# Optimization experiments

Hardware: AMD Instinct MI355X
Metric: run time of the kernel (lower is better)

The kernel has to match this reference:

```python
import jax, jax.numpy as jnp
import numpy as np

EPS = 1e-5  # torch BatchNorm default


def setup_inputs() -> dict:
    key = jax.random.key(0)
    k1, k2, k3 = jax.random.split(key, 3)
    N, C, T, V, O = 64, 64, 300, 25, 64
    x = jax.random.normal(k1, (N, C, T, V), dtype=jnp.float32)
    # 24 = V-1 convs, each (O, C, 1, 2) -> packed as (V-1, O, C, 2), scaled like conv_init
    W = jax.random.normal(k2, (V - 1, O, C, 2), dtype=jnp.float32) * (1.0 / np.sqrt(2 * C))
    b = jax.random.normal(k3, (V - 1, O), dtype=jnp.float32) * 0.01
    gamma = jnp.ones((O,), dtype=jnp.float32)
    beta = jnp.zeros((O,), dtype=jnp.float32)
    return {"x": x, "W": W, "b": b, "gamma": gamma, "beta": beta}


def reference(x, W, b, gamma, beta):
    # x: (N, C, T, V); W: (V-1, O, C, 2); b: (V-1, O)
    # Math of the original loop: out[..., v] = sum_i W0_i @ x[..., v]
    #   + sum_i W1_i @ x[..., (v+i+1) % V] + sum_i b_i
    V = x.shape[-1]
    W0 = W[..., 0]  # (V-1, O, C)
    W1 = W[..., 1]  # (V-1, O, C)
    # identity-tap term: all W0 share the same column -> sum once
    S0 = W0.sum(axis=0)  # (O, C)
    out = jnp.einsum('oc,nctv->notv', S0, x)
    # circular term: source u = (v+i+1)%V  <=>  i = (u-v-1)%V, valid for u != v
    v_idx = jnp.arange(V)
    off = (v_idx[None, :] - v_idx[:, None] - 1) % V  # (V_target, V_source) -> i, equals V-1 when u==v
    W1p = jnp.concatenate([W1, jnp.zeros_like(W1[:1])], axis=0)  # index V-1 maps to zero (u==v excluded)
    Wg = W1p[off]  # (V, V, O, C), zero on the diagonal
    out = out + jnp.einsum('vuoc,nctu->notv', Wg, x)
    out = out + b.sum(axis=0)[None, :, None, None]
    # BatchNorm2d (training-mode batch stats, biased variance) + ReLU
    mean = out.mean(axis=(0, 2, 3), keepdims=True)
    var = out.var(axis=(0, 2, 3), keepdims=True)
    out = (out - mean) * jax.lax.rsqrt(var + EPS)
    out = out * gamma[None, :, None, None] + beta[None, :, None, None]
    return jax.nn.relu(out)
```

## Files before the change

### kernel.cpp

```cpp
#include <hip/hip_runtime.h>


typedef short  s16x8 __attribute__((ext_vector_type(8)));
typedef float  f32x4 __attribute__((ext_vector_type(4)));

#define NTHR_   256
#define RPB_    250
#define NBR_    30
#define TS_     260

__device__ __forceinline__ unsigned short f2bf(float f) {
  unsigned u = __builtin_bit_cast(unsigned, f);
  return (unsigned short)((u + 0x7FFFu + ((u >> 16) & 1u)) >> 16);
}

__global__ void pack_w_kernel(const float* __restrict__ W, s16x8* __restrict__ Wg) {
  int idx = blockIdx.x * 256 + threadIdx.x;
  if (idx >= 12800) return;
  int lane  = idx & 63;
  int ni    = (idx >> 6) & 3;
  int chunk = (idx >> 8) & 1;
  int s     = idx >> 9;
  int o     = (ni << 4) + (lane & 15);
  int cbase = (chunk << 5) + ((lane >> 4) << 3);
  s16x8 h;
#pragma unroll
  for (int j = 0; j < 8; ++j) {
    int c = cbase + j;
    float val;
    if (s == 0) {
      val = 0.f;
      for (int i = 0; i < 24; ++i) val += W[((i * 64 + o) * 64 + c) * 2];
    } else {
      val = W[(((s - 1) * 64 + o) * 64 + c) * 2 + 1];
    }
    h[j] = (short)f2bf(val);
  }
  Wg[idx] = h;
}

#define ADV(J) { bool w_ = (u[J] == 24); u[J] = w_ ? 0 : u[J] + 1; \
                 aoc[J] += w_ ? -384 : 16; }
#define MM(RT, CT, AF, BF) \
  acc[RT][CT] = __builtin_amdgcn_mfma_f32_16x16x32_bf16(AF, BF, acc[RT][CT], 0, 0, 0);

#define SHIFT(S_, BB)                                                          \
  {                                                                            \
    int sc_ = (S_) + 2; sc_ = (sc_ > 24) ? 24 : sc_;                           \
    const s16x8* ws_ = Wg + sc_ * 512;                                         \
    s16x8 Br0_ = ws_[tid], Br1_ = ws_[256 + tid];                              \
    const char* bq_ = Bsh + (BB) * 8192 + 4096 + (lane << 4);                  \
    __builtin_amdgcn_s_setprio(1);                                             \
    Aq0 = *(const s16x8*)(Ash + aoc[0] + 16384);                               \
    MM(0, 0, Ap0, Bp0) MM(0, 1, Ap0, Bp1)                                      \
    Bq0 = *(const s16x8*)(bq_);                                                \
    MM(0, 2, Ap0, Bp2) MM(0, 3, Ap0, Bp3)                                      \
    Aq1 = *(const s16x8*)(Ash + aoc[1] + 16384);                               \
    MM(1, 0, Ap1, Bp0) MM(1, 1, Ap1, Bp1)                                      \
    Bq1 = *(const s16x8*)(bq_ + 1024);                                         \
    MM(1, 2, Ap1, Bp2) MM(1, 3, Ap1, Bp3)                                      \
    Aq2 = *(const s16x8*)(Ash + aoc[2] + 16384);                               \
    MM(2, 0, Ap2, Bp0) MM(2, 1, Ap2, Bp1)                                      \
    Bq2 = *(const s16x8*)(bq_ + 2048);                                         \
    MM(2, 2, Ap2, Bp2) MM(2, 3, Ap2, Bp3)                                      \
    Aq3 = *(const s16x8*)(Ash + aoc[3] + 16384);                               \
    MM(3, 0, Ap3, Bp0) MM(3, 1, Ap3, Bp1)                                      \
    Bq3 = *(const s16x8*)(bq_ + 3072);                                         \
    MM(3, 2, Ap3, Bp2) MM(3, 3, Ap3, Bp3)                                      \
    __builtin_amdgcn_s_setprio(0);                                             \
    __syncthreads();                                                           \
    const char* bp_ = Bsh + (((BB) ^ 1) * 8192) + (lane << 4);                 \
    __builtin_amdgcn_s_setprio(1);                                             \
    ADV(0) Ap0 = *(const s16x8*)(Ash + aoc[0]);                                \
    MM(0, 0, Aq0, Bq0) MM(0, 1, Aq0, Bq1)                                      \
    Bp0 = *(const s16x8*)(bp_);                                                \
    MM(0, 2, Aq0, Bq2) MM(0, 3, Aq0, Bq3)                                      \
    ADV(1) Ap1 = *(const s16x8*)(Ash + aoc[1]);                                \
    MM(1, 0, Aq1, Bq0) MM(1, 1, Aq1, Bq1)                                      \
    Bp1 = *(const s16x8*)(bp_ + 1024);                                         \
    MM(1, 2, Aq1, Bq2) MM(1, 3, Aq1, Bq3)                                      \
    ADV(2) Ap2 = *(const s16x8*)(Ash + aoc[2]);                                \
    MM(2, 0, Aq2, Bq0) MM(2, 1, Aq2, Bq1)                                      \
    Bp2 = *(const s16x8*)(bp_ + 2048);                                         \
    MM(2, 2, Aq2, Bq2) MM(2, 3, Aq2, Bq3)                                      \
    ADV(3) Ap3 = *(const s16x8*)(Ash + aoc[3]);                                \
    MM(3, 0, Aq3, Bq0) MM(3, 1, Aq3, Bq1)                                      \
    Bp3 = *(const s16x8*)(bp_ + 3072);                                         \
    MM(3, 2, Aq3, Bq2) MM(3, 3, Aq3, Bq3)                                      \
    __builtin_amdgcn_s_setprio(0);                                             \
    *(s16x8*)(Bsh + (BB) * 8192 + (tid << 4)) = Br0_;                          \
    *(s16x8*)(Bsh + (BB) * 8192 + 4096 + (tid << 4)) = Br1_;                   \
  }

__global__ __launch_bounds__(NTHR_) void tap_mm_kernel(
    const float* __restrict__ x, const s16x8* __restrict__ Wg,
    float* __restrict__ out, float* __restrict__ partials) {
  __shared__ __align__(16) char Ash[32768];
  __shared__ __align__(16) char Bsh[16384];
  float* red2 = (float*)Bsh;
  int br = blockIdx.x, n = blockIdx.y;
  int r0 = br * RPB_;
  const float* xn = x + n * 480000 + r0;
  int tid = threadIdx.x;
  int wid = tid >> 6, lane = tid & 63;
  int l15 = lane & 15, lk = lane >> 4;

  s16x8 p0 = Wg[tid], p1 = Wg[256 + tid], p2 = Wg[512 + tid], p3 = Wg[768 + tid];

#pragma unroll 2
  for (int it = 0; it < 8; ++it) {
    bool vld = tid < RPB_;
    s16x8 h;
#pragma unroll
    for (int j = 0; j < 8; ++j) {
      float f = vld ? xn[((it << 3) + j) * 7500 + tid] : 0.f;
      h[j] = (short)f2bf(f);
    }
    *(s16x8*)(Ash + (it << 12) + (tid << 4)) = h;
  }
  *(s16x8*)(Bsh + (tid << 4))         = p0;
  *(s16x8*)(Bsh + 4096 + (tid << 4))  = p1;
  *(s16x8*)(Bsh + 8192 + (tid << 4))  = p2;
  *(s16x8*)(Bsh + 12288 + (tid << 4)) = p3;

  int u[4], aoc[4];
#pragma unroll
  for (int rt = 0; rt < 4; ++rt) {
    int srow = (wid << 6) + (rt << 4) + l15;
    u[rt]   = srow % 25;
    aoc[rt] = (lk << 12) + (srow << 4);
  }
  f32x4 acc[4][4];
#pragma unroll
  for (int rt = 0; rt < 4; ++rt)
#pragma unroll
    for (int ct = 0; ct < 4; ++ct) acc[rt][ct] = (f32x4){0.f, 0.f, 0.f, 0.f};

  __syncthreads();

  s16x8 Ap0 = *(const s16x8*)(Ash + aoc[0]);
  s16x8 Ap1 = *(const s16x8*)(Ash + aoc[1]);
  s16x8 Ap2 = *(const s16x8*)(Ash + aoc[2]);
  s16x8 Ap3 = *(const s16x8*)(Ash + aoc[3]);
  const char* b0_ = Bsh + (lane << 4);
  s16x8 Bp0 = *(const s16x8*)(b0_);
  s16x8 Bp1 = *(const s16x8*)(b0_ + 1024);
  s16x8 Bp2 = *(const s16x8*)(b0_ + 2048);
  s16x8 Bp3 = *(const s16x8*)(b0_ + 3072);
  s16x8 Aq0, Aq1, Aq2, Aq3, Bq0, Bq1, Bq2, Bq3;

  for (int k = 0; k < 12; ++k) {
    SHIFT(2 * k, 0)
    SHIFT(2 * k + 1, 1)
  }
  SHIFT(24, 0)

  __syncthreads();

  float s1v[4] = {0.f, 0.f, 0.f, 0.f}, s2v[4] = {0.f, 0.f, 0.f, 0.f};
#pragma unroll
  for (int rt = 0; rt < 4; ++rt) {
#pragma unroll
    for (int qq = 0; qq < 4; ++qq) {
      int rloc = (wid << 6) + (rt << 4) + (lk << 2) + qq;
      if (rloc < RPB_) {
#pragma unroll
        for (int ct = 0; ct < 4; ++ct) {
          float val = acc[rt][ct][qq];
          s1v[ct] += val;
          s2v[ct] += val * val;
        }
      }
    }
  }
#pragma unroll
  for (int ct = 0; ct < 4; ++ct) {
    float a = s1v[ct], b = s2v[ct];
    a += __shfl_xor(a, 16); a += __shfl_xor(a, 32);
    b += __shfl_xor(b, 16); b += __shfl_xor(b, 32);
    if (lane < 16) {
      int base = ((((wid << 2) + ct) << 4) + l15) * 2;
      red2[base]     = a;
      red2[base + 1] = b;
    }
  }

  float* T = (float*)Ash;
  float* outb = out + n * 480000 + r0;
#pragma unroll
  for (int qt = 0; qt < 4; ++qt) {
    __syncthreads();
#pragma unroll
    for (int rt = 0; rt < 4; ++rt) {
      int row0 = (wid << 6) + (rt << 4) + (lk << 2);
      *(f32x4*)&T[l15 * TS_ + row0] = acc[rt][qt];
    }
    __syncthreads();
    if (qt == 0 && tid < 128) {
      int o = tid >> 1, m = tid & 1;
      int ct = o >> 4, ol = o & 15;
      float sres = 0.f;
#pragma unroll
      for (int w = 0; w < 4; ++w)
        sres += red2[((((w << 2) + ct) << 4) + ol) * 2 + m];
      int bl = n * NBR_ + br;
      partials[bl * 128 + m * 64 + o] = sres;
    }
#pragma unroll
    for (int it = 0; it < 8; ++it) {
      int idx = tid + it * NTHR_;
      if (idx < 2000) {
        int ol = idx / 125, r2 = idx - ol * 125;
        *(float2*)&outb[((qt << 4) + ol) * 7500 + (r2 << 1)] =
            *(float2*)&T[ol * TS_ + (r2 << 1)];
      }
    }
  }
}

__global__ void finalize_kernel(const float* __restrict__ part,
                                const float* __restrict__ gamma,
                                const float* __restrict__ beta,
                                float* __restrict__ scsh) {
  __shared__ float sm[512];
  int o = blockIdx.x;
  int tid = threadIdx.x;
  float s1 = 0.f, s2 = 0.f;
  for (int b = tid; b < 64 * NBR_; b += 256) {
    s1 += part[b * 128 + o];
    s2 += part[b * 128 + 64 + o];
  }
  sm[tid] = s1; sm[256 + tid] = s2;
  __syncthreads();
  for (int st = 128; st >= 1; st >>= 1) {
    if (tid < st) { sm[tid] += sm[tid + st]; sm[256 + tid] += sm[256 + tid + st]; }
    __syncthreads();
  }
  if (tid == 0) {
    const float inv = 1.0f / 480000.0f;
    float mean = sm[0] * inv;
    float var  = sm[256] * inv - mean * mean;
    float sc = gamma[o] * rsqrtf(var + 1e-5f);
    float sh = beta[o] - mean * sc;
    scsh[o]      = sc;
    scsh[64 + o] = sh;
  }
}

__global__ void bn_relu_kernel(float4* __restrict__ out, const float* __restrict__ scsh) {
  int i = blockIdx.x * blockDim.x + threadIdx.x;
  const int total = 7680000;
  int stride = gridDim.x * blockDim.x;
  for (; i < total; i += stride) {
    int o = (i / 1875) & 63;
    float sc = scsh[o], sh = scsh[64 + o];
    float4 v = out[i];
    v.x = fmaxf(fmaf(v.x, sc, sh), 0.f);
    v.y = fmaxf(fmaf(v.y, sc, sh), 0.f);
    v.z = fmaxf(fmaf(v.z, sc, sh), 0.f);
    v.w = fmaxf(fmaf(v.w, sc, sh), 0.f);
    out[i] = v;
  }
}

extern "C" void kernel_launch(void* const* d_in, const int* in_sizes, int n_in,
                              void* d_out, int out_size, void* d_ws, size_t ws_size,
                              hipStream_t stream) {
  const float* x     = (const float*)d_in[0];
  const float* W     = (const float*)d_in[1];
  const float* gamma = (const float*)d_in[3];
  const float* beta  = (const float*)d_in[4];
  float* out = (float*)d_out;

  char* ws = (char*)d_ws;
  s16x8* Wg       = (s16x8*)ws;
  float* partials = (float*)(ws + 204800);
  float* scsh     = (float*)(ws + 204800 + 983040);

  pack_w_kernel<<<dim3(50), dim3(256), 0, stream>>>(W, Wg);
  tap_mm_kernel<<<dim3(NBR_, 64), dim3(NTHR_), 0, stream>>>(x, Wg, out, partials);
  finalize_kernel<<<dim3(64), dim3(256), 0, stream>>>(partials, gamma, beta, scsh);
  bn_relu_kernel<<<dim3(2048), dim3(256), 0, stream>>>((float4*)out, scsh);
}
```

Before: 178.5 us.

## Switch tap GEMM to 32x32x16 bf16 MFMA tiles with repacked weights

```diff
diff --git a/kernel.cpp b/kernel.cpp
--- a/kernel.cpp
+++ b/kernel.cpp
@@ -1,13 +1,14 @@
 #include <hip/hip_runtime.h>
 
 
-typedef short  s16x8 __attribute__((ext_vector_type(8)));
-typedef float  f32x4 __attribute__((ext_vector_type(4)));
+typedef short  s16x8  __attribute__((ext_vector_type(8)));
+typedef float  f32x4  __attribute__((ext_vector_type(4)));
+typedef float  f32x16 __attribute__((ext_vector_type(16)));
 
 #define NTHR_   256
 #define RPB_    250
 #define NBR_    30
-#define TS_     260
+#define TS_     252
 
 __device__ __forceinline__ unsigned short f2bf(float f) {
   unsigned u = __builtin_bit_cast(unsigned, f);
@@ -17,22 +18,23 @@
 __global__ void pack_w_kernel(const float* __restrict__ W, s16x8* __restrict__ Wg) {
   int idx = blockIdx.x * 256 + threadIdx.x;
   if (idx >= 12800) return;
-  int lane  = idx & 63;
-  int ni    = (idx >> 6) & 3;
-  int chunk = (idx >> 8) & 1;
-  int s     = idx >> 9;
-  int o     = (ni << 4) + (lane & 15);
-  int cbase = (chunk << 5) + ((lane >> 4) << 3);
+  int lane = idx & 63;
+  int rest = idx >> 6;
+  int ct   = rest & 1;
+  int ks   = (rest >> 1) & 3;
+  int s    = rest >> 3;
+  int o    = (ct << 5) + (lane & 31);
+  int kb   = (ks << 4) + ((lane >> 5) << 3);
   s16x8 h;
 #pragma unroll
   for (int j = 0; j < 8; ++j) {
-    int c = cbase + j;
+    int k = kb + j;
     float val;
     if (s == 0) {
       val = 0.f;
-      for (int i = 0; i < 24; ++i) val += W[((i * 64 + o) * 64 + c) * 2];
+      for (int i = 0; i < 24; ++i) val += W[((i * 64 + o) * 64 + k) * 2];
     } else {
-      val = W[(((s - 1) * 64 + o) * 64 + c) * 2 + 1];
+      val = W[(((s - 1) * 64 + o) * 64 + k) * 2 + 1];
     }
     h[j] = (short)f2bf(val);
   }
@@ -41,52 +43,54 @@
 
 #define ADV(J) { bool w_ = (u[J] == 24); u[J] = w_ ? 0 : u[J] + 1; \
                  aoc[J] += w_ ? -384 : 16; }
-#define MM(RT, CT, AF, BF) \
-  acc[RT][CT] = __builtin_amdgcn_mfma_f32_16x16x32_bf16(AF, BF, acc[RT][CT], 0, 0, 0);
-
-#define SHIFT(S_, BB)                                                          \
+#define MM32(RT, CT, AF, BF) \
+  acc[RT][CT] = __builtin_amdgcn_mfma_f32_32x32x16_bf16(AF, BF, acc[RT][CT], 0, 0, 0);
+
+#define SHIFT32(S_, BB)                                                        \
   {                                                                            \
     int sc_ = (S_) + 2; sc_ = (sc_ > 24) ? 24 : sc_;                           \
     const s16x8* ws_ = Wg + sc_ * 512;                                         \
     s16x8 Br0_ = ws_[tid], Br1_ = ws_[256 + tid];                              \
     const char* bq_ = Bsh + (BB) * 8192 + 4096 + (lane << 4);                  \
     __builtin_amdgcn_s_setprio(1);                                             \
-    Aq0 = *(const s16x8*)(Ash + aoc[0] + 16384);                               \
-    MM(0, 0, Ap0, Bp0) MM(0, 1, Ap0, Bp1)                                      \
-    Bq0 = *(const s16x8*)(bq_);                                                \
-    MM(0, 2, Ap0, Bp2) MM(0, 3, Ap0, Bp3)                                      \
-    Aq1 = *(const s16x8*)(Ash + aoc[1] + 16384);                               \
-    MM(1, 0, Ap1, Bp0) MM(1, 1, Ap1, Bp1)                                      \
-    Bq1 = *(const s16x8*)(bq_ + 1024);                                         \
-    MM(1, 2, Ap1, Bp2) MM(1, 3, Ap1, Bp3)                                      \
-    Aq2 = *(const s16x8*)(Ash + aoc[2] + 16384);                               \
-    MM(2, 0, Ap2, Bp0) MM(2, 1, Ap2, Bp1)                                      \
-    Bq2 = *(const s16x8*)(bq_ + 2048);                                         \
-    MM(2, 2, Ap2, Bp2) MM(2, 3, Ap2, Bp3)                                      \
-    Aq3 = *(const s16x8*)(Ash + aoc[3] + 16384);                               \
-    MM(3, 0, Ap3, Bp0) MM(3, 1, Ap3, Bp1)                                      \
-    Bq3 = *(const s16x8*)(bq_ + 3072);                                         \
-    MM(3, 2, Ap3, Bp2) MM(3, 3, Ap3, Bp3)                                      \
+    Ra00 = *(const s16x8*)(Ash + aoc[0] + 16384);                              \
+    MM32(0, 0, Qa00, Qb00)                                                     \
+    Ra10 = *(const s16x8*)(Ash + aoc[1] + 16384);                              \
+    MM32(1, 0, Qa10, Qb00)                                                     \
+    Ra01 = *(const s16x8*)(Ash + aoc[0] + 24576);                              \
+    MM32(0, 1, Qa00, Qb01)                                                     \
+    Ra11 = *(const s16x8*)(Ash + aoc[1] + 24576);                              \
+    MM32(1, 1, Qa10, Qb01)                                                     \
+    Rb00 = *(const s16x8*)(bq_);                                               \
+    MM32(0, 0, Qa01, Qb10)                                                     \
+    Rb01 = *(const s16x8*)(bq_ + 1024);                                        \
+    MM32(0, 1, Qa01, Qb11)                                                     \
+    Rb10 = *(const s16x8*)(bq_ + 2048);                                        \
+    MM32(1, 0, Qa11, Qb10)                                                     \
+    Rb11 = *(const s16x8*)(bq_ + 3072);                                        \
+    MM32(1, 1, Qa11, Qb11)                                                     \
     __builtin_amdgcn_s_setprio(0);                                             \
     __syncthreads();                                                           \
     const char* bp_ = Bsh + (((BB) ^ 1) * 8192) + (lane << 4);                 \
     __builtin_amdgcn_s_setprio(1);                                             \
-    ADV(0) Ap0 = *(const s16x8*)(Ash + aoc[0]);                                \
-    MM(0, 0, Aq0, Bq0) MM(0, 1, Aq0, Bq1)                                      \
-    Bp0 = *(const s16x8*)(bp_);                                                \
-    MM(0, 2, Aq0, Bq2) MM(0, 3, Aq0, Bq3)                                      \
-    ADV(1) Ap1 = *(const s16x8*)(Ash + aoc[1]);                                \
-    MM(1, 0, Aq1, Bq0) MM(1, 1, Aq1, Bq1)                                      \
-    Bp1 = *(const s16x8*)(bp_ + 1024);                                         \
-    MM(1, 2, Aq1, Bq2) MM(1, 3, Aq1, Bq3)                                      \
-    ADV(2) Ap2 = *(const s16x8*)(Ash + aoc[2]);                                \
-    MM(2, 0, Aq2, Bq0) MM(2, 1, Aq2, Bq1)                                      \
-    Bp2 = *(const s16x8*)(bp_ + 2048);                                         \
-    MM(2, 2, Aq2, Bq2) MM(2, 3, Aq2, Bq3)                                      \
-    ADV(3) Ap3 = *(const s16x8*)(Ash + aoc[3]);                                \
-    MM(3, 0, Aq3, Bq0) MM(3, 1, Aq3, Bq1)                                      \
-    Bp3 = *(const s16x8*)(bp_ + 3072);                                         \
-    MM(3, 2, Aq3, Bq2) MM(3, 3, Aq3, Bq3)                                      \
+    ADV(0)                                                                     \
+    Qa00 = *(const s16x8*)(Ash + aoc[0]);                                      \
+    MM32(0, 0, Ra00, Rb00)                                                     \
+    ADV(1)                                                                     \
+    Qa10 = *(const s16x8*)(Ash + aoc[1]);                                      \
+    MM32(1, 0, Ra10, Rb00)                                                     \
+    Qa01 = *(const s16x8*)(Ash + aoc[0] + 8192);                               \
+    MM32(0, 1, Ra00, Rb01)                                                     \
+    Qa11 = *(const s16x8*)(Ash + aoc[1] + 8192);                               \
+    MM32(1, 1, Ra10, Rb01)                                                     \
+    Qb00 = *(const s16x8*)(bp_);                                               \
+    MM32(0, 0, Ra01, Rb10)                                                     \
+    Qb01 = *(const s16x8*)(bp_ + 1024);                                        \
+    MM32(0, 1, Ra01, Rb11)                                                     \
+    Qb10 = *(const s16x8*)(bp_ + 2048);                                        \
+    MM32(1, 0, Ra11, Rb10)                                                     \
+    Qb11 = *(const s16x8*)(bp_ + 3072);                                        \
+    MM32(1, 1, Ra11, Rb11)                                                     \
     __builtin_amdgcn_s_setprio(0);                                             \
     *(s16x8*)(Bsh + (BB) * 8192 + (tid << 4)) = Br0_;                          \
     *(s16x8*)(Bsh + (BB) * 8192 + 4096 + (tid << 4)) = Br1_;                   \
@@ -103,7 +107,7 @@
   const float* xn = x + n * 480000 + r0;
   int tid = threadIdx.x;
   int wid = tid >> 6, lane = tid & 63;
-  int l15 = lane & 15, lk = lane >> 4;
+  int l31 = lane & 31, hi = lane >> 5;
 
   s16x8 p0 = Wg[tid], p1 = Wg[256 + tid], p2 = Wg[512 + tid], p3 = Wg[768 + tid];
 
@@ -123,95 +127,95 @@
   *(s16x8*)(Bsh + 8192 + (tid << 4))  = p2;
   *(s16x8*)(Bsh + 12288 + (tid << 4)) = p3;
 
-  int u[4], aoc[4];
-#pragma unroll
-  for (int rt = 0; rt < 4; ++rt) {
-    int srow = (wid << 6) + (rt << 4) + l15;
+  int u[2], aoc[2];
+#pragma unroll
+  for (int rt = 0; rt < 2; ++rt) {
+    int srow = (wid << 6) + (rt << 5) + l31;
     u[rt]   = srow % 25;
-    aoc[rt] = (lk << 12) + (srow << 4);
-  }
-  f32x4 acc[4][4];
-#pragma unroll
-  for (int rt = 0; rt < 4; ++rt)
-#pragma unroll
-    for (int ct = 0; ct < 4; ++ct) acc[rt][ct] = (f32x4){0.f, 0.f, 0.f, 0.f};
+    aoc[rt] = (hi << 12) + (srow << 4);
+  }
+  f32x16 acc[2][2];
+#pragma unroll
+  for (int rt = 0; rt < 2; ++rt)
+#pragma unroll
+    for (int ct = 0; ct < 2; ++ct) acc[rt][ct] = (f32x16)(0.f);
 
   __syncthreads();
 
-  s16x8 Ap0 = *(const s16x8*)(Ash + aoc[0]);
-  s16x8 Ap1 = *(const s16x8*)(Ash + aoc[1]);
-  s16x8 Ap2 = *(const s16x8*)(Ash + aoc[2]);
-  s16x8 Ap3 = *(const s16x8*)(Ash + aoc[3]);
+  s16x8 Qa00 = *(const s16x8*)(Ash + aoc[0]);
+  s16x8 Qa10 = *(const s16x8*)(Ash + aoc[1]);
+  s16x8 Qa01 = *(const s16x8*)(Ash + aoc[0] + 8192);
+  s16x8 Qa11 = *(const s16x8*)(Ash + aoc[1] + 8192);
   const char* b0_ = Bsh + (lane << 4);
-  s16x8 Bp0 = *(const s16x8*)(b0_);
-  s16x8 Bp1 = *(const s16x8*)(b0_ + 1024);
-  s16x8 Bp2 = *(const s16x8*)(b0_ + 2048);
-  s16x8 Bp3 = *(const s16x8*)(b0_ + 3072);
-  s16x8 Aq0, Aq1, Aq2, Aq3, Bq0, Bq1, Bq2, Bq3;
+  s16x8 Qb00 = *(const s16x8*)(b0_);
+  s16x8 Qb01 = *(const s16x8*)(b0_ + 1024);
+  s16x8 Qb10 = *(const s16x8*)(b0_ + 2048);
+  s16x8 Qb11 = *(const s16x8*)(b0_ + 3072);
+  s16x8 Ra00, Ra10, Ra01, Ra11, Rb00, Rb01, Rb10, Rb11;
 
   for (int k = 0; k < 12; ++k) {
-    SHIFT(2 * k, 0)
-    SHIFT(2 * k + 1, 1)
-  }
-  SHIFT(24, 0)
+    SHIFT32(2 * k, 0)
+    SHIFT32(2 * k + 1, 1)
+  }
+  SHIFT32(24, 0)
 
   __syncthreads();
 
-  float s1v[4] = {0.f, 0.f, 0.f, 0.f}, s2v[4] = {0.f, 0.f, 0.f, 0.f};
-#pragma unroll
-  for (int rt = 0; rt < 4; ++rt) {
-#pragma unroll
-    for (int qq = 0; qq < 4; ++qq) {
-      int rloc = (wid << 6) + (rt << 4) + (lk << 2) + qq;
-      if (rloc < RPB_) {
-#pragma unroll
-        for (int ct = 0; ct < 4; ++ct) {
-          float val = acc[rt][ct][qq];
-          s1v[ct] += val;
-          s2v[ct] += val * val;
+  float s1v[2] = {0.f, 0.f}, s2v[2] = {0.f, 0.f};
+#pragma unroll
+  for (int rt = 0; rt < 2; ++rt)
+#pragma unroll
+    for (int r = 0; r < 16; ++r) {
+      int row = (wid << 6) + (rt << 5) + (r & 3) + ((r >> 2) << 3) + (hi << 2);
+      if (row < RPB_) {
+        float v0 = acc[rt][0][r], v1 = acc[rt][1][r];
+        s1v[0] += v0; s2v[0] += v0 * v0;
+        s1v[1] += v1; s2v[1] += v1 * v1;
+      }
+    }
+#pragma unroll
+  for (int ct = 0; ct < 2; ++ct) {
+    float a = s1v[ct], b = s2v[ct];
+    a += __shfl_xor(a, 32); b += __shfl_xor(b, 32);
+    if (lane < 32) {
+      int base = ((((wid << 1) + ct) << 5) + l31) * 2;
+      red2[base]     = a;
+      red2[base + 1] = b;
+    }
+  }
+
+  float* T = (float*)Ash;
+  float* outb = out + n * 480000 + r0;
+#pragma unroll
+  for (int ct = 0; ct < 2; ++ct) {
+    __syncthreads();
+#pragma unroll
+    for (int rt = 0; rt < 2; ++rt)
+#pragma unroll
+      for (int q = 0; q < 4; ++q) {
+        int trow = (wid << 6) + (rt << 5) + (q << 3) + (hi << 2);
+        if (trow < RPB_) {
+          f32x4 v = {acc[rt][ct][4 * q],     acc[rt][ct][4 * q + 1],
+                     acc[rt][ct][4 * q + 2], acc[rt][ct][4 * q + 3]};
+          *(f32x4*)&T[l31 * TS_ + trow] = v;
         }
       }
-    }
-  }
-#pragma unroll
-  for (int ct = 0; ct < 4; ++ct) {
-    float a = s1v[ct], b = s2v[ct];
-    a += __shfl_xor(a, 16); a += __shfl_xor(a, 32);
-    b += __shfl_xor(b, 16); b += __shfl_xor(b, 32);
-    if (lane < 16) {
-      int base = ((((wid << 2) + ct) << 4) + l15) * 2;
-      red2[base]     = a;
-      red2[base + 1] = b;
-    }
-  }
-
-  float* T = (float*)Ash;
-  float* outb = out + n * 480000 + r0;
-#pragma unroll
-  for (int qt = 0; qt < 4; ++qt) {
     __syncthreads();
-#pragma unroll
-    for (int rt = 0; rt < 4; ++rt) {
-      int row0 = (wid << 6) + (rt << 4) + (lk << 2);
-      *(f32x4*)&T[l15 * TS_ + row0] = acc[rt][qt];
-    }
-    __syncthreads();
-    if (qt == 0 && tid < 128) {
+    if (ct == 0 && tid < 128) {
       int o = tid >> 1, m = tid & 1;
-      int ct = o >> 4, ol = o & 15;
       float sres = 0.f;
 #pragma unroll
       for (int w = 0; w < 4; ++w)
-        sres += red2[((((w << 2) + ct) << 4) + ol) * 2 + m];
+        sres += red2[((((w << 1) + (o >> 5)) << 5) + (o & 31)) * 2 + m];
       int bl = n * NBR_ + br;
       partials[bl * 128 + m * 64 + o] = sres;
     }
-#pragma unroll
-    for (int it = 0; it < 8; ++it) {
+#pragma unroll 4
+    for (int it = 0; it < 16; ++it) {
       int idx = tid + it * NTHR_;
-      if (idx < 2000) {
+      if (idx < 4000) {
         int ol = idx / 125, r2 = idx - ol * 125;
-        *(float2*)&outb[((qt << 4) + ol) * 7500 + (r2 << 1)] =
+        *(float2*)&outb[((ct << 5) + ol) * 7500 + (r2 << 1)] =
             *(float2*)&T[ol * TS_ + (r2 << 1)];
       }
     }
```

Measured after the change: 189.0 us. 5.9% more time.
